# Optimization experiments

Hardware: AMD Instinct MI355X
Metric: run time of the kernel (lower is better)

## Reference

```python
import jax, jax.numpy as jnp
import numpy as np

B, S, L = 8, 64, 6          # graphs, spatial side, orientation layers
K = 6                       # Chebyshev order
IN_D, HID, OUT_D = 3, 128, 10


def _grid_edges(num_graphs, s, l):
    b, o, y, x = np.meshgrid(np.arange(num_graphs), np.arange(l), np.arange(s), np.arange(s), indexing='ij')
    nid = ((b * l + o) * s + y) * s + x  # linear node id, [B,L,s,s]
    srcs, dsts = [], []
    def add(a, c):
        srcs.append(a.ravel()); dsts.append(c.ravel())
    add(nid[..., :-1], nid[..., 1:]); add(nid[..., 1:], nid[..., :-1])                 # x-neighbors
    add(nid[:, :, :-1, :], nid[:, :, 1:, :]); add(nid[:, :, 1:, :], nid[:, :, :-1, :])  # y-neighbors
    nxt = np.roll(nid, -1, axis=1)                                                     # orientation ring
    add(nid, nxt); add(nxt, nid)
    return np.stack([np.concatenate(srcs), np.concatenate(dsts)]).astype(np.int32)


def _cluster_spatial(num_graphs, s, l):
    b, o, y, x = np.meshgrid(np.arange(num_graphs), np.arange(l), np.arange(s), np.arange(s), indexing='ij')
    h = s // 2
    return (((b * l + o) * h + y // 2) * h + x // 2).ravel().astype(np.int32)


def setup_inputs() -> dict:
    key = jax.random.key(0)
    ks = jax.random.split(key, 20)
    inp = {}
    N1 = B * L * S * S
    inp['x'] = jax.random.normal(ks[0], (N1, IN_D), jnp.float32)
    for i, s in enumerate([S, S // 2, S // 4]):
        ei = _grid_edges(B, s, L)
        inp[f'edge_index{i+1}'] = jnp.asarray(ei)
        inp[f'edge_attr{i+1}'] = jax.random.uniform(ks[1 + i], (ei.shape[1],), jnp.float32, 0.1, 1.0)
    inp['cluster1'] = jnp.asarray(_cluster_spatial(B, S, L))
    inp['cluster2'] = jnp.asarray(_cluster_spatial(B, S // 2, L))
    inp['cluster3'] = jnp.asarray(_cluster_spatial(B, S // 4, L))
    s4 = S // 8
    b, o, y, x = np.meshgrid(np.arange(B), np.arange(L), np.arange(s4), np.arange(s4), indexing='ij')
    inp['cluster4'] = jnp.asarray(((b * s4 + y) * s4 + x).ravel().astype(np.int32))  # collapse orientation axis
    inp['batch_final'] = jnp.asarray(np.repeat(np.arange(B), s4 * s4).astype(np.int32))
    dims = [(IN_D, HID), (HID, HID), (HID, HID), (HID, HID), (HID, HID), (HID, OUT_D)]
    for i, (di, do) in enumerate(dims):
        inp[f'W{i+1}'] = jax.random.normal(ks[8 + i], (K, di, do), jnp.float32) / np.float32(np.sqrt(di * K))
        inp[f'b{i+1}'] = jnp.zeros((do,), jnp.float32)
    for i in range(5):
        inp[f'gamma{i+1}'] = jnp.ones((HID,), jnp.float32)
        inp[f'beta{i+1}'] = jnp.zeros((HID,), jnp.float32)
    return inp


def _cheb_conv(x, ei, ea, W, b):
    # Chebyshev polynomial graph conv: out = sum_k T_k(L) x @ W_k + b,
    # with T0=x, T1=Lx, Tk = 2 L T_{k-1} - T_{k-2}; L applied via edge gather/scatter.
    src, dst = ei[0], ei[1]
    n = x.shape[0]
    def lap(v):
        return jax.ops.segment_sum(ea[:, None] * v[src], dst, num_segments=n)
    Tx0 = x
    out = Tx0 @ W[0]
    Tx1 = lap(x)
    out = out + Tx1 @ W[1]
    for k in range(2, W.shape[0]):
        Tx2 = 2.0 * lap(Tx1) - Tx0
        out = out + Tx2 @ W[k]
        Tx0, Tx1 = Tx1, Tx2
    return out + b


def _bn(x, g, bt):
    # BatchNorm1d in training mode (batch statistics, biased variance, eps=1e-5)
    mu = x.mean(0)
    var = x.var(0)
    return g * (x - mu) * jax.lax.rsqrt(var + 1e-5) + bt


def reference(x, edge_index1, edge_attr1, edge_index2, edge_attr2, edge_index3, edge_attr3, cluster1, cluster2, cluster3, cluster4, batch_final, W1, b1, W2, b2, W3, b3, W4, b4, W5, b5, W6, b6, gamma1, beta1, gamma2, beta2, gamma3, beta3, gamma4, beta4, gamma5, beta5):
    h = jax.nn.relu(_bn(_cheb_conv(x, edge_index1, edge_attr1, W1, b1), gamma1, beta1))
    h = jax.nn.relu(_bn(_cheb_conv(h, edge_index1, edge_attr1, W2, b2), gamma2, beta2))
    h = jax.ops.segment_max(h, cluster1, num_segments=B * L * (S // 2) ** 2)
    h = jax.nn.relu(_bn(_cheb_conv(h, edge_index2, edge_attr2, W3, b3), gamma3, beta3))
    h = jax.nn.relu(_bn(_cheb_conv(h, edge_index2, edge_attr2, W4, b4), gamma4, beta4))
    h = jax.ops.segment_max(h, cluster2, num_segments=B * L * (S // 4) ** 2)
    h = jax.nn.relu(_bn(_cheb_conv(h, edge_index3, edge_attr3, W5, b5), gamma5, beta5))
    h = jax.nn.relu(_cheb_conv(h, edge_index3, edge_attr3, W6, b6))
    h = jax.ops.segment_max(h, cluster3, num_segments=B * L * (S // 8) ** 2)   # spatial pool 3
    h = jax.ops.segment_max(h, cluster4, num_segments=B * (S // 8) ** 2)        # orientation pool
    g = jax.ops.segment_max(h, batch_final, num_segments=B)                     # global max pool
    return jax.nn.log_softmax(g, axis=1)
```

## Files before the change

kernel.cpp:

```cpp
#include <hip/hip_runtime.h>
#include <math.h>

#define L_OR 6
#define N_BL 48

typedef unsigned short u16;
typedef __attribute__((ext_vector_type(8))) short s8v;
typedef __attribute__((ext_vector_type(4))) float f4v;

#define N1 196608
#define N2 49152
#define N3 12288
#define LSTRIDE 114688

__device__ u16   g_cat[(size_t)N1 * 768 + 1024];
__device__ u16   g_O[(size_t)N1 * 128];
__device__ float g_Tt[5 * (size_t)N1 * 3];
__device__ u16   g_Bt[4 * LSTRIDE];
__device__ u16   g_W6t[16 * 768];
__device__ float g_wt1[(size_t)N1 * 8];
__device__ float g_wt2[(size_t)N2 * 8];
__device__ float g_wt3[(size_t)N3 * 8];
__device__ float g_O10[(size_t)N3 * 10];
__device__ float g_part[1536 * 256];
__device__ float g_part2[64 * 256];
__device__ float g_gsc[128];
__device__ float g_gso[128];

__device__ __forceinline__ float b2f(u16 v) {
    return __uint_as_float(((unsigned)v) << 16);
}
__device__ __forceinline__ u16 f2b(float f) {
    unsigned u = __float_as_uint(f);
    return (u16)((u + 0x7FFFu + ((u >> 16) & 1u)) >> 16);
}

__global__ __launch_bounds__(256)
void eaprep_all(float* __restrict__ wt1, float* __restrict__ wt2,
                float* __restrict__ wt3, const float* __restrict__ ea1,
                const float* __restrict__ ea2, const float* __restrict__ ea3)
{
    int idx = blockIdx.x * 256 + threadIdx.x;
    int S, n; float* wtab; const float* ea;
    if (idx < N1)            { S = 64; wtab = wt1; ea = ea1; n = idx; }
    else if (idx < N1 + N2)  { S = 32; wtab = wt2; ea = ea2; n = idx - N1; }
    else if (idx < N1 + N2 + N3) { S = 16; wtab = wt3; ea = ea3; n = idx - N1 - N2; }
    else return;
    int x = n % S, y = (n / S) % S, g = n / (S * S);
    int o = g % L_OR, b = g / L_OR;
    const int szx = N_BL * S * (S - 1);
    const int basex = (g * S + y) * (S - 1);
    float wxm = (x > 0)     ? ea[basex + x - 1] : 0.f;
    float wxp = (x < S - 1) ? ea[szx + basex + x] : 0.f;
    float wym = (y > 0)     ? ea[2 * szx + (g * (S - 1) + y - 1) * S + x] : 0.f;
    float wyp = (y < S - 1) ? ea[3 * szx + (g * (S - 1) + y) * S + x] : 0.f;
    int op_ = (o == 0) ? L_OR - 1 : o - 1;
    int on_ = (o == L_OR - 1) ? 0 : o + 1;
    int sp = ((b * L_OR + op_) * S + y) * S + x;
    int sn = ((b * L_OR + on_) * S + y) * S + x;
    float wom = ea[4 * szx + sp];
    float wop = ea[4 * szx + N_BL * S * S + n];
    float* w = wtab + (size_t)n * 8;
    w[0] = wxm; w[1] = wxp; w[2] = wym; w[3] = wyp; w[4] = wom; w[5] = wop;
    ((int*)w)[6] = sp - n;
    ((int*)w)[7] = sn - n;
}

template<int S>
__global__ __launch_bounds__(256)
void lap128b(u16* __restrict__ cat, int outSlot, int inSlot, int tppSlot,
             const float* __restrict__ wtab, float alpha)
{
    const int NN = N_BL * S * S;
    int node = blockIdx.x * 16 + (threadIdx.x >> 4);
    int c8   = threadIdx.x & 15;

    float4 wa = *(const float4*)(wtab + (size_t)node * 8);
    float4 wb = *(const float4*)(wtab + (size_t)node * 8 + 4);
    int dsp = __float_as_int(wb.z);
    int dsn = __float_as_int(wb.w);
    int sxm = (node > 0)      ? node - 1 : 0;
    int sxp = (node < NN - 1) ? node + 1 : node;
    int sym = (node >= S)     ? node - S : node;
    int syp = (node < NN - S) ? node + S : node;

    const int chOff = inSlot * 128 + c8 * 8;
    float a[8] = {0.f, 0.f, 0.f, 0.f, 0.f, 0.f, 0.f, 0.f};
    auto gather = [&](int src, float w) {
        s8v v = *(const s8v*)(cat + (size_t)src * 768 + chOff);
#pragma unroll
        for (int j = 0; j < 8; ++j) a[j] += w * b2f((u16)v[j]);
    };
    gather(sxm, wa.x); gather(sxp, wa.y); gather(sym, wa.z); gather(syp, wa.w);
    gather(node + dsp, wb.x); gather(node + dsn, wb.y);

    float r[8];
#pragma unroll
    for (int j = 0; j < 8; ++j) r[j] = alpha * a[j];
    if (tppSlot >= 0) {
        s8v t = *(const s8v*)(cat + (size_t)node * 768 + tppSlot * 128 + c8 * 8);
#pragma unroll
        for (int j = 0; j < 8; ++j) r[j] -= b2f((u16)t[j]);
    }
    uint4 ov;
    asm("v_cvt_pk_bf16_f32 %0, %1, %2" : "=v"(ov.x) : "v"(r[0]), "v"(r[1]));
    asm("v_cvt_pk_bf16_f32 %0, %1, %2" : "=v"(ov.y) : "v"(r[2]), "v"(r[3]));
    asm("v_cvt_pk_bf16_f32 %0, %1, %2" : "=v"(ov.z) : "v"(r[4]), "v"(r[5]));
    asm("v_cvt_pk_bf16_f32 %0, %1, %2" : "=v"(ov.w) : "v"(r[6]), "v"(r[7]));
    *(uint4*)(cat + (size_t)node * 768 + outSlot * 128 + c8 * 8) = ov;
}

template<int S>
__global__ __launch_bounds__(256)
void lap1bn(u16* __restrict__ cat, const u16* __restrict__ O,
            int t0Slot, int t1Slot, const float* __restrict__ wtab,
            const float* __restrict__ gsc, const float* __restrict__ gso)
{
    const int NN = N_BL * S * S;
    int node = blockIdx.x * 16 + (threadIdx.x >> 4);
    int c8   = threadIdx.x & 15;

    float4 wa = *(const float4*)(wtab + (size_t)node * 8);
    float4 wb = *(const float4*)(wtab + (size_t)node * 8 + 4);
    int dsp = __float_as_int(wb.z);
    int dsn = __float_as_int(wb.w);
    int sxm = (node > 0)      ? node - 1 : 0;
    int sxp = (node < NN - 1) ? node + 1 : node;
    int sym = (node >= S)     ? node - S : node;
    int syp = (node < NN - S) ? node + S : node;

    float sc[8], so[8];
    {
        float4 s0 = *(const float4*)(gsc + c8 * 8);
        float4 s1 = *(const float4*)(gsc + c8 * 8 + 4);
        float4 o0 = *(const float4*)(gso + c8 * 8);
        float4 o1 = *(const float4*)(gso + c8 * 8 + 4);
        sc[0]=s0.x; sc[1]=s0.y; sc[2]=s0.z; sc[3]=s0.w;
        sc[4]=s1.x; sc[5]=s1.y; sc[6]=s1.z; sc[7]=s1.w;
        so[0]=o0.x; so[1]=o0.y; so[2]=o0.z; so[3]=o0.w;
        so[4]=o1.x; so[5]=o1.y; so[6]=o1.z; so[7]=o1.w;
    }

    float a[8] = {0.f, 0.f, 0.f, 0.f, 0.f, 0.f, 0.f, 0.f};
    auto gatherbn = [&](int src, float w) {
        s8v v = *(const s8v*)(O + (size_t)src * 128 + c8 * 8);
#pragma unroll
        for (int j = 0; j < 8; ++j)
            a[j] += w * fmaxf(b2f((u16)v[j]) * sc[j] + so[j], 0.f);
    };
    gatherbn(sxm, wa.x); gatherbn(sxp, wa.y); gatherbn(sym, wa.z); gatherbn(syp, wa.w);
    gatherbn(node + dsp, wb.x); gatherbn(node + dsn, wb.y);

    float t0[8];
    {
        s8v v = *(const s8v*)(O + (size_t)node * 128 + c8 * 8);
#pragma unroll
        for (int j = 0; j < 8; ++j)
            t0[j] = fmaxf(b2f((u16)v[j]) * sc[j] + so[j], 0.f);
    }
    uint4 o0v, o1v;
    asm("v_cvt_pk_bf16_f32 %0, %1, %2" : "=v"(o0v.x) : "v"(t0[0]), "v"(t0[1]));
    asm("v_cvt_pk_bf16_f32 %0, %1, %2" : "=v"(o0v.y) : "v"(t0[2]), "v"(t0[3]));
    asm("v_cvt_pk_bf16_f32 %0, %1, %2" : "=v"(o0v.z) : "v"(t0[4]), "v"(t0[5]));
    asm("v_cvt_pk_bf16_f32 %0, %1, %2" : "=v"(o0v.w) : "v"(t0[6]), "v"(t0[7]));
    asm("v_cvt_pk_bf16_f32 %0, %1, %2" : "=v"(o1v.x) : "v"(a[0]), "v"(a[1]));
    asm("v_cvt_pk_bf16_f32 %0, %1, %2" : "=v"(o1v.y) : "v"(a[2]), "v"(a[3]));
    asm("v_cvt_pk_bf16_f32 %0, %1, %2" : "=v"(o1v.z) : "v"(a[4]), "v"(a[5]));
    asm("v_cvt_pk_bf16_f32 %0, %1, %2" : "=v"(o1v.w) : "v"(a[6]), "v"(a[7]));
    *(uint4*)(cat + (size_t)node * 768 + t0Slot * 128 + c8 * 8) = o0v;
    *(uint4*)(cat + (size_t)node * 768 + t1Slot * 128 + c8 * 8) = o1v;
}

template<int S>
__global__ __launch_bounds__(256)
void lap3_kernel(float* __restrict__ out, const float* __restrict__ in,
                 const float* __restrict__ tpp, const float* __restrict__ wtab,
                 float alpha)
{
    const int NN = N_BL * S * S;
    int n = blockIdx.x * 256 + threadIdx.x;
    if (n >= NN) return;
    float4 wa = *(const float4*)(wtab + (size_t)n * 8);
    float4 wb = *(const float4*)(wtab + (size_t)n * 8 + 4);
    int dsp = __float_as_int(wb.z);
    int dsn = __float_as_int(wb.w);
    int sxm = (n > 0)      ? n - 1 : 0;
    int sxp = (n < NN - 1) ? n + 1 : n;
    int sym = (n >= S)     ? n - S : n;
    int syp = (n < NN - S) ? n + S : n;

    float a0 = 0.f, a1 = 0.f, a2 = 0.f;
    auto gather = [&](int src, float w) {
        a0 += w * in[src * 3 + 0];
        a1 += w * in[src * 3 + 1];
        a2 += w * in[src * 3 + 2];
    };
    gather(sxm, wa.x); gather(sxp, wa.y); gather(sym, wa.z); gather(syp, wa.w);
    gather(n + dsp, wb.x); gather(n + dsn, wb.y);

    float r0 = alpha * a0, r1 = alpha * a1, r2 = alpha * a2;
    if (tpp) { r0 -= tpp[n * 3 + 0]; r1 -= tpp[n * 3 + 1]; r2 -= tpp[n * 3 + 2]; }
    out[n * 3 + 0] = r0; out[n * 3 + 1] = r1; out[n * 3 + 2] = r2;
}

__global__ __launch_bounds__(256)
void gemm_mfma_cat(u16* __restrict__ O, const u16* __restrict__ A,
                   const u16* __restrict__ Bf, const float* __restrict__ bias,
                   float* __restrict__ partials)
{
    __shared__ u16 Bs[2][8192];
    const int tid  = threadIdx.x;
    const int wave = tid >> 6;
    const int lane = tid & 63;
    const int lrow = lane & 15;
    const int kg   = lane >> 4;
    const int r0   = blockIdx.x * 128 + wave * 32;

    const u16* A0 = A + (size_t)(r0 + lrow) * 768 + kg * 8;
    const u16* A1 = A0 + (size_t)16 * 768;

    f4v acc[2][8] = {};

#define COMPUTE(BUF, A00, A10, A01, A11)                                        \
    {                                                                           \
        _Pragma("unroll")                                                       \
        for (int ct = 0; ct < 8; ++ct) {                                        \
            s8v b = *(const s8v*)&Bs[BUF][(ct * 64 + lane) * 8];                \
            acc[0][ct] = __builtin_amdgcn_mfma_f32_16x16x32_bf16(A00, b, acc[0][ct], 0, 0, 0); \
            acc[1][ct] = __builtin_amdgcn_mfma_f32_16x16x32_bf16(A10, b, acc[1][ct], 0, 0, 0); \
        }                                                                       \
        _Pragma("unroll")                                                       \
        for (int ct = 0; ct < 8; ++ct) {                                        \
            s8v b = *(const s8v*)&Bs[BUF][4096 + (ct * 64 + lane) * 8];         \
            acc[0][ct] = __builtin_amdgcn_mfma_f32_16x16x32_bf16(A01, b, acc[0][ct], 0, 0, 0); \
            acc[1][ct] = __builtin_amdgcn_mfma_f32_16x16x32_bf16(A11, b, acc[1][ct], 0, 0, 0); \
        }                                                                       \
    }

#pragma unroll
    for (int i = 0; i < 4; ++i)
        *(s8v*)&Bs[0][i * 2048 + tid * 8] = *(const s8v*)(Bf + i * 2048 + tid * 8);
    s8v rX0 = *(const s8v*)(Bf + 8192 + tid * 8);
    s8v rX1 = *(const s8v*)(Bf + 8192 + 2048 + tid * 8);
    s8v rX2 = *(const s8v*)(Bf + 8192 + 4096 + tid * 8);
    s8v rX3 = *(const s8v*)(Bf + 8192 + 6144 + tid * 8);
    s8v a00 = *(const s8v*)(A0);
    s8v a10 = *(const s8v*)(A1);
    s8v a01 = *(const s8v*)(A0 + 32);
    s8v a11 = *(const s8v*)(A1 + 32);
    s8v rY0, rY1, rY2, rY3;
    __syncthreads();

#pragma unroll 1
    for (int q = 0; q < 6; ++q) {
        {
            const int p = 2 * q;
            const u16* src = Bf + (p + 2) * 8192;
            rY0 = *(const s8v*)(src + tid * 8);
            rY1 = *(const s8v*)(src + 2048 + tid * 8);
            rY2 = *(const s8v*)(src + 4096 + tid * 8);
            rY3 = *(const s8v*)(src + 6144 + tid * 8);
            s8v na00 = *(const s8v*)(A0 + (p + 1) * 64);
            s8v na10 = *(const s8v*)(A1 + (p + 1) * 64);
            s8v na01 = *(const s8v*)(A0 + (p + 1) * 64 + 32);
            s8v na11 = *(const s8v*)(A1 + (p + 1) * 64 + 32);
            COMPUTE(0, a00, a10, a01, a11);
            __syncthreads();
            *(s8v*)&Bs[1][tid * 8]        = rX0;
            *(s8v*)&Bs[1][2048 + tid * 8] = rX1;
            *(s8v*)&Bs[1][4096 + tid * 8] = rX2;
            *(s8v*)&Bs[1][6144 + tid * 8] = rX3;
            __syncthreads();
            a00 = na00; a10 = na10; a01 = na01; a11 = na11;
        }
        {
            const int p = 2 * q + 1;
            const u16* src = Bf + (p + 2) * 8192;
            rX0 = *(const s8v*)(src + tid * 8);
            rX1 = *(const s8v*)(src + 2048 + tid * 8);
            rX2 = *(const s8v*)(src + 4096 + tid * 8);
            rX3 = *(const s8v*)(src + 6144 + tid * 8);
            s8v na00 = *(const s8v*)(A0 + (p + 1) * 64);
            s8v na10 = *(const s8v*)(A1 + (p + 1) * 64);
            s8v na01 = *(const s8v*)(A0 + (p + 1) * 64 + 32);
            s8v na11 = *(const s8v*)(A1 + (p + 1) * 64 + 32);
            COMPUTE(1, a00, a10, a01, a11);
            __syncthreads();
            *(s8v*)&Bs[0][tid * 8]        = rY0;
            *(s8v*)&Bs[0][2048 + tid * 8] = rY1;
            *(s8v*)&Bs[0][4096 + tid * 8] = rY2;
            *(s8v*)&Bs[0][6144 + tid * 8] = rY3;
            __syncthreads();
            a00 = na00; a10 = na10; a01 = na01; a11 = na11;
        }
    }
#undef COMPUTE

    __shared__ float sred[4][2][8][16];
    float cs[8], cq[8];
#pragma unroll
    for (int ct = 0; ct < 8; ++ct) { cs[ct] = 0.f; cq[ct] = 0.f; }

#pragma unroll
    for (int s = 0; s < 2; ++s)
#pragma unroll
        for (int ct = 0; ct < 8; ++ct) {
            int col = ct * 16 + lrow;
            float bv = bias[col];
#pragma unroll
            for (int j = 0; j < 4; ++j) {
                int row = r0 + s * 16 + kg * 4 + j;
                float v = acc[s][ct][j] + bv;
                O[(size_t)row * 128 + col] = f2b(v);
                cs[ct] += v; cq[ct] += v * v;
            }
        }
#pragma unroll
    for (int ct = 0; ct < 8; ++ct) {
        cs[ct] += __shfl_xor(cs[ct], 16); cs[ct] += __shfl_xor(cs[ct], 32);
        cq[ct] += __shfl_xor(cq[ct], 16); cq[ct] += __shfl_xor(cq[ct], 32);
    }
    if (lane < 16) {
#pragma unroll
        for (int ct = 0; ct < 8; ++ct) {
            sred[wave][0][ct][lane] = cs[ct];
            sred[wave][1][ct][lane] = cq[ct];
        }
    }
    __syncthreads();
    if (threadIdx.x < 128) {
        int ct = threadIdx.x >> 4, lr = threadIdx.x & 15;
        float S = 0.f, Q = 0.f;
#pragma unroll
        for (int w = 0; w < 4; ++w) { S += sred[w][0][ct][lr]; Q += sred[w][1][ct][lr]; }
        partials[blockIdx.x * 256 + threadIdx.x]       = S;
        partials[blockIdx.x * 256 + 128 + threadIdx.x] = Q;
    }
}

__global__ __launch_bounds__(256)
void wprep_all(const float* __restrict__ W2, const float* __restrict__ W3,
               const float* __restrict__ W4, const float* __restrict__ W5,
               u16* __restrict__ Bf)
{
    int l = blockIdx.y;
    const float* W = (l == 0) ? W2 : (l == 1) ? W3 : (l == 2) ? W4 : W5;
    int base = (l & 1) ? 5 : 0;
    int idx = blockIdx.x * 256 + threadIdx.x;
    int j    = idx & 7;
    int lane = (idx >> 3) & 63;
    int ct   = (idx >> 9) & 7;
    int k0s  = idx >> 12;
    int k    = k0s * 32 + (lane >> 4) * 8 + j;
    int col  = ct * 16 + (lane & 15);
    int slot = k >> 7, d = k & 127;
    int wk = slot - base; if (wk < 0) wk += 6;
    Bf[(size_t)l * LSTRIDE + idx] = f2b(W[(size_t)wk * 16384 + d * 128 + col]);
}

__global__ __launch_bounds__(256)
void w6prep(const float* __restrict__ W, u16* __restrict__ W6t, int base)
{
    int idx = blockIdx.x * 256 + threadIdx.x;
    if (idx >= 16 * 768) return;
    int c = idx / 768, kk = idx % 768;
    int slot = kk >> 7, d = kk & 127;
    int wk = slot - base; if (wk < 0) wk += 6;
    W6t[idx] = (c < 10) ? f2b(W[(size_t)wk * 1280 + d * 10 + c]) : (u16)0;
}

__global__ __launch_bounds__(256)
void l1gemm(u16* __restrict__ O, const float* __restrict__ T0,
            const float* __restrict__ Tt, const float* __restrict__ W,
            const float* __restrict__ bias, float* __restrict__ partials)
{
    __shared__ float Ts[128][18];
    __shared__ float sh[2][128], sh2[2][128];
    int tid = threadIdx.x;
    int rbase = blockIdx.x * 128;
    for (int i = tid; i < 128 * 18; i += 256) {
        int r = i / 18, t = i % 18;
        int k = t / 3, j = t % 3;
        Ts[r][t] = (k == 0) ? T0[(size_t)(rbase + r) * 3 + j]
                            : Tt[(size_t)(k - 1) * N1 * 3 + (size_t)(rbase + r) * 3 + j];
    }
    __syncthreads();
    int c = tid & 127, h = tid >> 7;
    float w[18];
#pragma unroll
    for (int k = 0; k < 6; ++k)
#pragma unroll
        for (int j = 0; j < 3; ++j) w[k * 3 + j] = W[(size_t)k * 384 + j * 128 + c];
    float bv = bias[c];
    float S = 0.f, Q = 0.f;
    for (int i = 0; i < 64; ++i) {
        int r = h * 64 + i;
        float acc = bv;
#pragma unroll
        for (int t = 0; t < 18; ++t) acc += Ts[r][t] * w[t];
        O[(size_t)(rbase + r) * 128 + c] = f2b(acc);
        S += acc; Q += acc * acc;
    }
    sh[h][c] = S; sh2[h][c] = Q;
    __syncthreads();
    if (tid < 128) {
        partials[blockIdx.x * 256 + tid]       = sh[0][tid] + sh[1][tid];
        partials[blockIdx.x * 256 + 128 + tid] = sh2[0][tid] + sh2[1][tid];
    }
}

__global__ __launch_bounds__(256)
void out10_cat(float* __restrict__ O10, const u16* __restrict__ cat,
               const u16* __restrict__ W6t, const float* __restrict__ bias)
{
    int col = threadIdx.x & 15;
    int row = blockIdx.x * 16 + (threadIdx.x >> 4);
    const u16* a = cat + (size_t)row * 768;
    const u16* w = W6t + (size_t)col * 768;
    float acc = 0.f;
#pragma unroll 4
    for (int k0 = 0; k0 < 768; k0 += 8) {
        s8v av = *(const s8v*)(a + k0);
        s8v wv = *(const s8v*)(w + k0);
#pragma unroll
        for (int j = 0; j < 8; ++j)
            acc += b2f((u16)av[j]) * b2f((u16)wv[j]);
    }
    if (col < 10)
        O10[(size_t)row * 10 + col] = fmaxf(acc + bias[col], 0.f);
}

__global__ __launch_bounds__(256)
void bn_reduce1(const float* __restrict__ partials, int nblk,
                float* __restrict__ part2)
{
    int tid = threadIdx.x;
    float S = 0.f;
#pragma unroll 4
    for (int b = blockIdx.x; b < nblk; b += 64)
        S += partials[(size_t)b * 256 + tid];
    part2[blockIdx.x * 256 + tid] = S;
}

__global__ __launch_bounds__(256)
void bn_finalize2(const float* __restrict__ part2, int N,
                  const float* __restrict__ g, const float* __restrict__ bt,
                  float* __restrict__ gsc, float* __restrict__ gso)
{
    int tid = threadIdx.x;
    int c = tid & 127, h = tid >> 7;
    float S = 0.f, Q = 0.f;
#pragma unroll 8
    for (int b = h; b < 64; b += 2) {
        S += part2[b * 256 + c];
        Q += part2[b * 256 + 128 + c];
    }
    __shared__ float shS[2][128], shQ[2][128];
    shS[h][c] = S; shQ[h][c] = Q;
    __syncthreads();
    if (tid < 128) {
        float Sa = shS[0][tid] + shS[1][tid];
        float Qa = shQ[0][tid] + shQ[1][tid];
        float inv_n = 1.f / (float)N;
        float mu = Sa * inv_n;
        float var = Qa * inv_n - mu * mu;
        float is = rsqrtf(var + 1e-5f);
        float sc = is * g[tid];
        gsc[tid] = sc;
        gso[tid] = bt[tid] - mu * sc;
    }
}

__global__ __launch_bounds__(256)
void bn_apply_pool8(const u16* __restrict__ O, u16* __restrict__ cat, int outSlot,
                    int s, int Nout,
                    const float* __restrict__ gsc, const float* __restrict__ gso)
{
    int idx = blockIdx.x * 256 + threadIdx.x;
    if (idx >= Nout * 16) return;
    int c8 = idx & 15;
    int n2 = idx >> 4;
    int h  = s >> 1;
    int x2 = n2 % h;
    int y2 = (n2 / h) % h;
    int gg = n2 / (h * h);
    int base = (gg * s + 2 * y2) * s + 2 * x2;
    s8v v0 = *(const s8v*)(O + (size_t)base * 128 + c8 * 8);
    s8v v1 = *(const s8v*)(O + (size_t)(base + 1) * 128 + c8 * 8);
    s8v v2 = *(const s8v*)(O + (size_t)(base + s) * 128 + c8 * 8);
    s8v v3 = *(const s8v*)(O + (size_t)(base + s + 1) * 128 + c8 * 8);
    s8v ov;
#pragma unroll
    for (int j = 0; j < 8; ++j) {
        int c = c8 * 8 + j;
        float sc = gsc[c], so = gso[c];
        float m =          b2f((u16)v0[j]) * sc + so;
        m = fmaxf(m, b2f((u16)v1[j]) * sc + so);
        m = fmaxf(m, b2f((u16)v2[j]) * sc + so);
        m = fmaxf(m, b2f((u16)v3[j]) * sc + so);
        ov[j] = (short)f2b(fmaxf(m, 0.f));
    }
    *(s8v*)(cat + (size_t)n2 * 768 + outSlot * 128 + c8 * 8) = ov;
}

__global__ __launch_bounds__(512)
void tail_fused(const float* __restrict__ O10, float* __restrict__ out)
{
    __shared__ float p4[512][10];
    __shared__ float G[8][10];
    __shared__ float rowm[8], rowl[8];
    int t = threadIdx.x;
    for (int i = t; i < 5120; i += 512) {
        int c = i % 10, n = i / 10;
        int x = n & 7, y = (n >> 3) & 7, b = n >> 6;
        float m = -INFINITY;
        for (int o = 0; o < L_OR; ++o) {
            int base = ((b * L_OR + o) * 16 + 2 * y) * 16 + 2 * x;
            m = fmaxf(m, O10[(size_t)base * 10 + c]);
            m = fmaxf(m, O10[(size_t)(base + 1) * 10 + c]);
            m = fmaxf(m, O10[(size_t)(base + 16) * 10 + c]);
            m = fmaxf(m, O10[(size_t)(base + 17) * 10 + c]);
        }
        p4[n][c] = m;
    }
    __syncthreads();
    if (t < 80) {
        int b = t / 10, c = t % 10;
        float m = -INFINITY;
        for (int p = 0; p < 64; ++p) m = fmaxf(m, p4[b * 64 + p][c]);
        G[b][c] = m;
    }
    __syncthreads();
    if (t < 8) {
        float m = -INFINITY;
        for (int c = 0; c < 10; ++c) m = fmaxf(m, G[t][c]);
        float s = 0.f;
        for (int c = 0; c < 10; ++c) s += expf(G[t][c] - m);
        rowm[t] = m; rowl[t] = logf(s);
    }
    __syncthreads();
    if (t < 80) {
        int b = t / 10, c = t % 10;
        out[t] = G[b][c] - rowm[b] - rowl[b];
    }
}

static void launch_lapb(u16* cat, int os, int is, int ts, const float* wtab,
                        int S, int N, float alpha, hipStream_t st)
{
    dim3 grid(N / 16), block(256);
    if (S == 64)      hipLaunchKernelGGL(lap128b<64>, grid, block, 0, st, cat, os, is, ts, wtab, alpha);
    else if (S == 32) hipLaunchKernelGGL(lap128b<32>, grid, block, 0, st, cat, os, is, ts, wtab, alpha);
    else              hipLaunchKernelGGL(lap128b<16>, grid, block, 0, st, cat, os, is, ts, wtab, alpha);
}

static void cheb_laps_b5(u16* cat, const float* wtab, int S, int N, hipStream_t st)
{
    for (int k = 1; k < 6; ++k) {
        int os = (k + 5) % 6;
        int is = (k - 1 + 5) % 6;
        int ts = (k >= 2) ? (k - 2 + 5) % 6 : -1;
        launch_lapb(cat, os, is, ts, wtab, S, N, (k == 1) ? 1.f : 2.f, st);
    }
}

static void cheb_laps_2to5(u16* cat, const float* wtab, int S, int N, hipStream_t st)
{
    for (int k = 2; k < 6; ++k)
        launch_lapb(cat, k, k - 1, k - 2, wtab, S, N, 2.f, st);
}

static void launch_lap1bn(u16* cat, const u16* O, const float* wtab,
                          const float* gsc, const float* gso,
                          int S, int N, hipStream_t st)
{
    dim3 grid(N / 16), block(256);
    if (S == 64)      hipLaunchKernelGGL(lap1bn<64>, grid, block, 0, st, cat, O, 0, 1, wtab, gsc, gso);
    else if (S == 32) hipLaunchKernelGGL(lap1bn<32>, grid, block, 0, st, cat, O, 0, 1, wtab, gsc, gso);
    else              hipLaunchKernelGGL(lap1bn<16>, grid, block, 0, st, cat, O, 0, 1, wtab, gsc, gso);
}

static void bn_reduce(float* part, float* part2, int nblk, int N,
                      const float* g, const float* bt,
                      float* gsc, float* gso, hipStream_t st)
{
    hipLaunchKernelGGL(bn_reduce1, dim3(64), dim3(256), 0, st, part, nblk, part2);
    hipLaunchKernelGGL(bn_finalize2, dim3(1), dim3(256), 0, st, part2, N, g, bt, gsc, gso);
}

extern "C" void kernel_launch(void* const* d_in, const int* in_sizes, int n_in,
                              void* d_out, int out_size, void* d_ws, size_t ws_size,
                              hipStream_t stream)
{
    const float* x   = (const float*)d_in[0];
    const float* ea1 = (const float*)d_in[2];
    const float* ea2 = (const float*)d_in[4];
    const float* ea3 = (const float*)d_in[6];
    const float* W1  = (const float*)d_in[12];
    const float* b1  = (const float*)d_in[13];
    const float* W2  = (const float*)d_in[14];
    const float* b2  = (const float*)d_in[15];
    const float* W3  = (const float*)d_in[16];
    const float* b3  = (const float*)d_in[17];
    const float* W4  = (const float*)d_in[18];
    const float* b4  = (const float*)d_in[19];
    const float* W5  = (const float*)d_in[20];
    const float* b5  = (const float*)d_in[21];
    const float* W6  = (const float*)d_in[22];
    const float* b6  = (const float*)d_in[23];
    const float* g1  = (const float*)d_in[24];
    const float* be1 = (const float*)d_in[25];
    const float* g2  = (const float*)d_in[26];
    const float* be2 = (const float*)d_in[27];
    const float* g3  = (const float*)d_in[28];
    const float* be3 = (const float*)d_in[29];
    const float* g4  = (const float*)d_in[30];
    const float* be4 = (const float*)d_in[31];
    const float* g5  = (const float*)d_in[32];
    const float* be5 = (const float*)d_in[33];

    u16 *cat, *O, *Bt, *W6t;
    float *Tt, *O10, *part, *part2, *gsc, *gso, *wt1, *wt2, *wt3;
    if (hipGetSymbolAddress((void**)&cat, HIP_SYMBOL(g_cat)) != hipSuccess) return;
    if (hipGetSymbolAddress((void**)&O,   HIP_SYMBOL(g_O))   != hipSuccess) return;
    if (hipGetSymbolAddress((void**)&Tt,  HIP_SYMBOL(g_Tt))  != hipSuccess) return;
    if (hipGetSymbolAddress((void**)&Bt,  HIP_SYMBOL(g_Bt))  != hipSuccess) return;
    if (hipGetSymbolAddress((void**)&W6t, HIP_SYMBOL(g_W6t)) != hipSuccess) return;
    if (hipGetSymbolAddress((void**)&O10, HIP_SYMBOL(g_O10)) != hipSuccess) return;
    if (hipGetSymbolAddress((void**)&part,  HIP_SYMBOL(g_part))  != hipSuccess) return;
    if (hipGetSymbolAddress((void**)&part2, HIP_SYMBOL(g_part2)) != hipSuccess) return;
    if (hipGetSymbolAddress((void**)&gsc, HIP_SYMBOL(g_gsc)) != hipSuccess) return;
    if (hipGetSymbolAddress((void**)&gso, HIP_SYMBOL(g_gso)) != hipSuccess) return;
    if (hipGetSymbolAddress((void**)&wt1, HIP_SYMBOL(g_wt1)) != hipSuccess) return;
    if (hipGetSymbolAddress((void**)&wt2, HIP_SYMBOL(g_wt2)) != hipSuccess) return;
    if (hipGetSymbolAddress((void**)&wt3, HIP_SYMBOL(g_wt3)) != hipSuccess) return;

    dim3 blk(256);

    hipLaunchKernelGGL(eaprep_all, dim3((N1 + N2 + N3) / 256), blk, 0, stream,
                       wt1, wt2, wt3, ea1, ea2, ea3);
    hipLaunchKernelGGL(wprep_all, dim3(384, 4), blk, 0, stream, W2, W3, W4, W5, Bt);
    hipLaunchKernelGGL(w6prep, dim3(48), blk, 0, stream, W6, W6t, 0);

    {
        float* t1 = Tt;
        float* t2 = Tt + (size_t)N1 * 3;
        float* t3 = Tt + (size_t)2 * N1 * 3;
        float* t4 = Tt + (size_t)3 * N1 * 3;
        float* t5 = Tt + (size_t)4 * N1 * 3;
        dim3 gl((N1 + 255) / 256);
        hipLaunchKernelGGL(lap3_kernel<64>, gl, blk, 0, stream, t1, x,  (const float*)nullptr, wt1, 1.f);
        hipLaunchKernelGGL(lap3_kernel<64>, gl, blk, 0, stream, t2, t1, x,  wt1, 2.f);
        hipLaunchKernelGGL(lap3_kernel<64>, gl, blk, 0, stream, t3, t2, t1, wt1, 2.f);
        hipLaunchKernelGGL(lap3_kernel<64>, gl, blk, 0, stream, t4, t3, t2, wt1, 2.f);
        hipLaunchKernelGGL(lap3_kernel<64>, gl, blk, 0, stream, t5, t4, t3, wt1, 2.f);
        hipLaunchKernelGGL(l1gemm, dim3(N1 / 128), blk, 0, stream, O, x, Tt, W1, b1, part);
    }
    bn_reduce(part, part2, N1 / 128, N1, g1, be1, gsc, gso, stream);

    launch_lap1bn(cat, O, wt1, gsc, gso, 64, N1, stream);
    cheb_laps_2to5(cat, wt1, 64, N1, stream);
    hipLaunchKernelGGL(gemm_mfma_cat, dim3(N1 / 128), blk, 0, stream, O, cat, Bt, b2, part);
    bn_reduce(part, part2, N1 / 128, N1, g2, be2, gsc, gso, stream);
    hipLaunchKernelGGL(bn_apply_pool8, dim3(N2 / 16), blk, 0, stream,
                       O, cat, 5, 64, N2, gsc, gso);

    cheb_laps_b5(cat, wt2, 32, N2, stream);
    hipLaunchKernelGGL(gemm_mfma_cat, dim3(N2 / 128), blk, 0, stream, O, cat, Bt + 1 * LSTRIDE, b3, part);
    bn_reduce(part, part2, N2 / 128, N2, g3, be3, gsc, gso, stream);

    launch_lap1bn(cat, O, wt2, gsc, gso, 32, N2, stream);
    cheb_laps_2to5(cat, wt2, 32, N2, stream);
    hipLaunchKernelGGL(gemm_mfma_cat, dim3(N2 / 128), blk, 0, stream, O, cat, Bt + 2 * LSTRIDE, b4, part);
    bn_reduce(part, part2, N2 / 128, N2, g4, be4, gsc, gso, stream);
    hipLaunchKernelGGL(bn_apply_pool8, dim3(N3 / 16), blk, 0, stream,
                       O, cat, 5, 32, N3, gsc, gso);

    cheb_laps_b5(cat, wt3, 16, N3, stream);
    hipLaunchKernelGGL(gemm_mfma_cat, dim3(N3 / 128), blk, 0, stream, O, cat, Bt + 3 * LSTRIDE, b5, part);
    bn_reduce(part, part2, N3 / 128, N3, g5, be5, gsc, gso, stream);

    launch_lap1bn(cat, O, wt3, gsc, gso, 16, N3, stream);
    cheb_laps_2to5(cat, wt3, 16, N3, stream);
    hipLaunchKernelGGL(out10_cat, dim3(N3 / 16), blk, 0, stream, O10, cat, W6t, b6);

    hipLaunchKernelGGL(tail_fused, dim3(1), dim3(512), 0, stream, O10, (float*)d_out);
}
```

Before: 760.5 us.

## Deepen GEMM B-tile pipeline to four stages and fuse BN reduce kernels

The MFMA GEMM moves from a two-buffer, two-barrier-per-step scheme over 64-wide K chunks to a four-slot ring of 32-wide K chunks, prefetched four steps ahead with a single barrier per step. This aims to hide global load latency and cut synchronisation. Separately, the two-kernel BN reduction becomes one kernel: the last block to finish, found with an atomic counter, computes scale and shift, which removes five kernel launches. The trade-offs are more loop iterations with less work each, an extra barrier before the epilogue's shared-memory writes, and reliance on the counter being reset on every call.

```diff
diff --git a/kernel.cpp b/kernel.cpp
--- a/kernel.cpp
+++ b/kernel.cpp
@@ -26,6 +26,7 @@
 __device__ float g_part2[64 * 256];
 __device__ float g_gsc[128];
 __device__ float g_gso[128];
+__device__ unsigned g_cnt;
 
 __device__ __forceinline__ float b2f(u16 v) {
     return __uint_as_float(((unsigned)v) << 16);
@@ -208,7 +209,7 @@
                    const u16* __restrict__ Bf, const float* __restrict__ bias,
                    float* __restrict__ partials)
 {
-    __shared__ u16 Bs[2][8192];
+    __shared__ u16 Bs[4][4096];
     const int tid  = threadIdx.x;
     const int wave = tid >> 6;
     const int lane = tid & 63;
@@ -221,80 +222,34 @@
 
     f4v acc[2][8] = {};
 
-#define COMPUTE(BUF, A00, A10, A01, A11)                                        \
-    {                                                                           \
-        _Pragma("unroll")                                                       \
-        for (int ct = 0; ct < 8; ++ct) {                                        \
-            s8v b = *(const s8v*)&Bs[BUF][(ct * 64 + lane) * 8];                \
-            acc[0][ct] = __builtin_amdgcn_mfma_f32_16x16x32_bf16(A00, b, acc[0][ct], 0, 0, 0); \
-            acc[1][ct] = __builtin_amdgcn_mfma_f32_16x16x32_bf16(A10, b, acc[1][ct], 0, 0, 0); \
-        }                                                                       \
-        _Pragma("unroll")                                                       \
-        for (int ct = 0; ct < 8; ++ct) {                                        \
-            s8v b = *(const s8v*)&Bs[BUF][4096 + (ct * 64 + lane) * 8];         \
-            acc[0][ct] = __builtin_amdgcn_mfma_f32_16x16x32_bf16(A01, b, acc[0][ct], 0, 0, 0); \
-            acc[1][ct] = __builtin_amdgcn_mfma_f32_16x16x32_bf16(A11, b, acc[1][ct], 0, 0, 0); \
-        }                                                                       \
-    }
-
-#pragma unroll
-    for (int i = 0; i < 4; ++i)
-        *(s8v*)&Bs[0][i * 2048 + tid * 8] = *(const s8v*)(Bf + i * 2048 + tid * 8);
-    s8v rX0 = *(const s8v*)(Bf + 8192 + tid * 8);
-    s8v rX1 = *(const s8v*)(Bf + 8192 + 2048 + tid * 8);
-    s8v rX2 = *(const s8v*)(Bf + 8192 + 4096 + tid * 8);
-    s8v rX3 = *(const s8v*)(Bf + 8192 + 6144 + tid * 8);
-    s8v a00 = *(const s8v*)(A0);
-    s8v a10 = *(const s8v*)(A1);
-    s8v a01 = *(const s8v*)(A0 + 32);
-    s8v a11 = *(const s8v*)(A1 + 32);
-    s8v rY0, rY1, rY2, rY3;
+#pragma unroll
+    for (int i = 0; i < 4; ++i) {
+        *(s8v*)&Bs[i][tid * 8]        = *(const s8v*)(Bf + i * 4096 + tid * 8);
+        *(s8v*)&Bs[i][2048 + tid * 8] = *(const s8v*)(Bf + i * 4096 + 2048 + tid * 8);
+    }
+    s8v a0 = *(const s8v*)(A0);
+    s8v a1 = *(const s8v*)(A1);
     __syncthreads();
 
 #pragma unroll 1
-    for (int q = 0; q < 6; ++q) {
-        {
-            const int p = 2 * q;
-            const u16* src = Bf + (p + 2) * 8192;
-            rY0 = *(const s8v*)(src + tid * 8);
-            rY1 = *(const s8v*)(src + 2048 + tid * 8);
-            rY2 = *(const s8v*)(src + 4096 + tid * 8);
-            rY3 = *(const s8v*)(src + 6144 + tid * 8);
-            s8v na00 = *(const s8v*)(A0 + (p + 1) * 64);
-            s8v na10 = *(const s8v*)(A1 + (p + 1) * 64);
-            s8v na01 = *(const s8v*)(A0 + (p + 1) * 64 + 32);
-            s8v na11 = *(const s8v*)(A1 + (p + 1) * 64 + 32);
-            COMPUTE(0, a00, a10, a01, a11);
-            __syncthreads();
-            *(s8v*)&Bs[1][tid * 8]        = rX0;
-            *(s8v*)&Bs[1][2048 + tid * 8] = rX1;
-            *(s8v*)&Bs[1][4096 + tid * 8] = rX2;
-            *(s8v*)&Bs[1][6144 + tid * 8] = rX3;
-            __syncthreads();
-            a00 = na00; a10 = na10; a01 = na01; a11 = na11;
+    for (int p = 0; p < 24; ++p) {
+        const int pl = (p + 4 < 24) ? p + 4 : 23;
+        s8v nb0 = *(const s8v*)(Bf + pl * 4096 + tid * 8);
+        s8v nb1 = *(const s8v*)(Bf + pl * 4096 + 2048 + tid * 8);
+        s8v na0 = *(const s8v*)(A0 + (p + 1) * 32);
+        s8v na1 = *(const s8v*)(A1 + (p + 1) * 32);
+        const u16* bsl = &Bs[p & 3][0];
+#pragma unroll
+        for (int ct = 0; ct < 8; ++ct) {
+            s8v b = *(const s8v*)&bsl[(ct * 64 + lane) * 8];
+            acc[0][ct] = __builtin_amdgcn_mfma_f32_16x16x32_bf16(a0, b, acc[0][ct], 0, 0, 0);
+            acc[1][ct] = __builtin_amdgcn_mfma_f32_16x16x32_bf16(a1, b, acc[1][ct], 0, 0, 0);
         }
-        {
-            const int p = 2 * q + 1;
-            const u16* src = Bf + (p + 2) * 8192;
-            rX0 = *(const s8v*)(src + tid * 8);
-            rX1 = *(const s8v*)(src + 2048 + tid * 8);
-            rX2 = *(const s8v*)(src + 4096 + tid * 8);
-            rX3 = *(const s8v*)(src + 6144 + tid * 8);
-            s8v na00 = *(const s8v*)(A0 + (p + 1) * 64);
-            s8v na10 = *(const s8v*)(A1 + (p + 1) * 64);
-            s8v na01 = *(const s8v*)(A0 + (p + 1) * 64 + 32);
-            s8v na11 = *(const s8v*)(A1 + (p + 1) * 64 + 32);
-            COMPUTE(1, a00, a10, a01, a11);
-            __syncthreads();
-            *(s8v*)&Bs[0][tid * 8]        = rY0;
-            *(s8v*)&Bs[0][2048 + tid * 8] = rY1;
-            *(s8v*)&Bs[0][4096 + tid * 8] = rY2;
-            *(s8v*)&Bs[0][6144 + tid * 8] = rY3;
-            __syncthreads();
-            a00 = na00; a10 = na10; a01 = na01; a11 = na11;
-        }
-    }
-#undef COMPUTE
+        __syncthreads();
+        *(s8v*)&Bs[p & 3][tid * 8]        = nb0;
+        *(s8v*)&Bs[p & 3][2048 + tid * 8] = nb1;
+        a0 = na0; a1 = na1;
+    }
 
     __shared__ float sred[4][2][8][16];
     float cs[8], cq[8];
@@ -320,6 +275,7 @@
         cs[ct] += __shfl_xor(cs[ct], 16); cs[ct] += __shfl_xor(cs[ct], 32);
         cq[ct] += __shfl_xor(cq[ct], 16); cq[ct] += __shfl_xor(cq[ct], 32);
     }
+    __syncthreads();
     if (lane < 16) {
 #pragma unroll
         for (int ct = 0; ct < 8; ++ct) {
@@ -431,8 +387,10 @@
 }
 
 __global__ __launch_bounds__(256)
-void bn_reduce1(const float* __restrict__ partials, int nblk,
-                float* __restrict__ part2)
+void bn_reduce_f(const float* __restrict__ partials, int nblk, int N,
+                 const float* __restrict__ g, const float* __restrict__ bt,
+                 float* __restrict__ gsc, float* __restrict__ gso,
+                 float* __restrict__ part2, unsigned* __restrict__ cnt)
 {
     int tid = threadIdx.x;
     float S = 0.f;
@@ -440,35 +398,35 @@
     for (int b = blockIdx.x; b < nblk; b += 64)
         S += partials[(size_t)b * 256 + tid];
     part2[blockIdx.x * 256 + tid] = S;
-}
-
-__global__ __launch_bounds__(256)
-void bn_finalize2(const float* __restrict__ part2, int N,
-                  const float* __restrict__ g, const float* __restrict__ bt,
-                  float* __restrict__ gsc, float* __restrict__ gso)
-{
-    int tid = threadIdx.x;
+    __threadfence();
+    __syncthreads();
+    __shared__ int last;
+    if (tid == 0) last = (atomicAdd(cnt, 1u) == 63u) ? 1 : 0;
+    __syncthreads();
+    if (!last) return;
+    __threadfence();
     int c = tid & 127, h = tid >> 7;
-    float S = 0.f, Q = 0.f;
+    float Sa = 0.f, Qa = 0.f;
 #pragma unroll 8
     for (int b = h; b < 64; b += 2) {
-        S += part2[b * 256 + c];
-        Q += part2[b * 256 + 128 + c];
+        Sa += part2[b * 256 + c];
+        Qa += part2[b * 256 + 128 + c];
     }
     __shared__ float shS[2][128], shQ[2][128];
-    shS[h][c] = S; shQ[h][c] = Q;
+    shS[h][c] = Sa; shQ[h][c] = Qa;
     __syncthreads();
     if (tid < 128) {
-        float Sa = shS[0][tid] + shS[1][tid];
-        float Qa = shQ[0][tid] + shQ[1][tid];
+        float Sx = shS[0][tid] + shS[1][tid];
+        float Qx = shQ[0][tid] + shQ[1][tid];
         float inv_n = 1.f / (float)N;
-        float mu = Sa * inv_n;
-        float var = Qa * inv_n - mu * mu;
+        float mu = Sx * inv_n;
+        float var = Qx * inv_n - mu * mu;
         float is = rsqrtf(var + 1e-5f);
         float sc = is * g[tid];
         gsc[tid] = sc;
         gso[tid] = bt[tid] - mu * sc;
     }
+    if (tid == 0) *cnt = 0u;
 }
 
 __global__ __launch_bounds__(256)
@@ -578,14 +536,6 @@
     if (S == 64)      hipLaunchKernelGGL(lap1bn<64>, grid, block, 0, st, cat, O, 0, 1, wtab, gsc, gso);
     else if (S == 32) hipLaunchKernelGGL(lap1bn<32>, grid, block, 0, st, cat, O, 0, 1, wtab, gsc, gso);
     else              hipLaunchKernelGGL(lap1bn<16>, grid, block, 0, st, cat, O, 0, 1, wtab, gsc, gso);
-}
-
-static void bn_reduce(float* part, float* part2, int nblk, int N,
-                      const float* g, const float* bt,
-                      float* gsc, float* gso, hipStream_t st)
-{
-    hipLaunchKernelGGL(bn_reduce1, dim3(64), dim3(256), 0, st, part, nblk, part2);
-    hipLaunchKernelGGL(bn_finalize2, dim3(1), dim3(256), 0, st, part2, N, g, bt, gsc, gso);
 }
 
 extern "C" void kernel_launch(void* const* d_in, const int* in_sizes, int n_in,
@@ -621,6 +571,7 @@
 
     u16 *cat, *O, *Bt, *W6t;
     float *Tt, *O10, *part, *part2, *gsc, *gso, *wt1, *wt2, *wt3;
+    unsigned* cnt;
     if (hipGetSymbolAddress((void**)&cat, HIP_SYMBOL(g_cat)) != hipSuccess) return;
     if (hipGetSymbolAddress((void**)&O,   HIP_SYMBOL(g_O))   != hipSuccess) return;
     if (hipGetSymbolAddress((void**)&Tt,  HIP_SYMBOL(g_Tt))  != hipSuccess) return;
@@ -634,6 +585,7 @@
     if (hipGetSymbolAddress((void**)&wt1, HIP_SYMBOL(g_wt1)) != hipSuccess) return;
     if (hipGetSymbolAddress((void**)&wt2, HIP_SYMBOL(g_wt2)) != hipSuccess) return;
     if (hipGetSymbolAddress((void**)&wt3, HIP_SYMBOL(g_wt3)) != hipSuccess) return;
+    if (hipGetSymbolAddress((void**)&cnt, HIP_SYMBOL(g_cnt)) != hipSuccess) return;
 
     dim3 blk(256);
 
@@ -656,29 +608,34 @@
         hipLaunchKernelGGL(lap3_kernel<64>, gl, blk, 0, stream, t5, t4, t3, wt1, 2.f);
         hipLaunchKernelGGL(l1gemm, dim3(N1 / 128), blk, 0, stream, O, x, Tt, W1, b1, part);
     }
-    bn_reduce(part, part2, N1 / 128, N1, g1, be1, gsc, gso, stream);
+    hipLaunchKernelGGL(bn_reduce_f, dim3(64), blk, 0, stream, part, N1 / 128, N1,
+                       g1, be1, gsc, gso, part2, cnt);
 
     launch_lap1bn(cat, O, wt1, gsc, gso, 64, N1, stream);
     cheb_laps_2to5(cat, wt1, 64, N1, stream);
     hipLaunchKernelGGL(gemm_mfma_cat, dim3(N1 / 128), blk, 0, stream, O, cat, Bt, b2, part);
-    bn_reduce(part, part2, N1 / 128, N1, g2, be2, gsc, gso, stream);
+    hipLaunchKernelGGL(bn_reduce_f, dim3(64), blk, 0, stream, part, N1 / 128, N1,
+                       g2, be2, gsc, gso, part2, cnt);
     hipLaunchKernelGGL(bn_apply_pool8, dim3(N2 / 16), blk, 0, stream,
                        O, cat, 5, 64, N2, gsc, gso);
 
     cheb_laps_b5(cat, wt2, 32, N2, stream);
     hipLaunchKernelGGL(gemm_mfma_cat, dim3(N2 / 128), blk, 0, stream, O, cat, Bt + 1 * LSTRIDE, b3, part);
-    bn_reduce(part, part2, N2 / 128, N2, g3, be3, gsc, gso, stream);
+    hipLaunchKernelGGL(bn_reduce_f, dim3(64), blk, 0, stream, part, N2 / 128, N2,
+                       g3, be3, gsc, gso, part2, cnt);
 
     launch_lap1bn(cat, O, wt2, gsc, gso, 32, N2, stream);
     cheb_laps_2to5(cat, wt2, 32, N2, stream);
     hipLaunchKernelGGL(gemm_mfma_cat, dim3(N2 / 128), blk, 0, stream, O, cat, Bt + 2 * LSTRIDE, b4, part);
-    bn_reduce(part, part2, N2 / 128, N2, g4, be4, gsc, gso, stream);
+    hipLaunchKernelGGL(bn_reduce_f, dim3(64), blk, 0, stream, part, N2 / 128, N2,
+                       g4, be4, gsc, gso, part2, cnt);
     hipLaunchKernelGGL(bn_apply_pool8, dim3(N3 / 16), blk, 0, stream,
                        O, cat, 5, 32, N3, gsc, gso);
 
     cheb_laps_b5(cat, wt3, 16, N3, stream);
     hipLaunchKernelGGL(gemm_mfma_cat, dim3(N3 / 128), blk, 0, stream, O, cat, Bt + 3 * LSTRIDE, b5, part);
-    bn_reduce(part, part2, N3 / 128, N3, g5, be5, gsc, gso, stream);
+    hipLaunchKernelGGL(bn_reduce_f, dim3(64), blk, 0, stream, part, N3 / 128, N3,
+                       g5, be5, gsc, gso, part2, cnt);
 
     launch_lap1bn(cat, O, wt3, gsc, gso, 16, N3, stream);
     cheb_laps_2to5(cat, wt3, 16, N3, stream);
```

Measured after the change: 787.7 us. 1.04x slower.
